# Optimization experiments

Hardware: AMD Instinct MI355X
Metric: run time of the kernel (lower is better)

## Reference

```python
import jax, jax.numpy as jnp
import numpy as np

# ---- configuration matching init_kwargs ----
CTX_C = 96        # context_v_features
M_FREQS = 8       # m_encode_num_freqs
OUT_C = 45        # out_features
NDIM = 3
SIGMA = 5.0       # sigma_encode_scale
EPS = 1e-7        # TARGET_COORD_EPSILON
CX = CY = CZ = 32
QX = QY = QZ = 48
B = 1
CTX_VOX = 2.0
Q_VOX = 1.25
N_COORD = 4 * NDIM + NDIM * 2 * M_FREQS   # 60
INTERNAL = CTX_C + N_COORD                # 156


def _lin_init(k, fi, fo):
    s = 1.0 / np.sqrt(fi)
    kw, kb = jax.random.split(k)
    return (jax.random.uniform(kw, (fi, fo), jnp.float32, -s, s),
            jax.random.uniform(kb, (fo,), jnp.float32, -s, s))


def setup_inputs() -> dict:
    key = jax.random.key(0)
    ks = jax.random.split(key, 12)
    context_v = jax.random.normal(ks[0], (B, CTX_C, CX, CY, CZ), jnp.float32)
    ax = jnp.arange(CX, dtype=jnp.float32) * CTX_VOX
    gx, gy, gz = jnp.meshgrid(ax, ax, ax, indexing='ij')
    context_spatial_extent = jnp.broadcast_to(
        jnp.stack([gx, gy, gz], 0)[None], (B, 3, CX, CY, CZ)).astype(jnp.float32)
    # queries in the interior so nearest-idx + 1 stays in bounds
    query_coord = jax.random.uniform(ks[1], (B, 3, QX, QY, QZ), jnp.float32,
                                     CTX_VOX, (CX - 2) * CTX_VOX)
    query_vox_size = jnp.full((B, 3), Q_VOX, jnp.float32)
    inp = dict(context_v=context_v, context_spatial_extent=context_spatial_extent,
               query_vox_size=query_vox_size, query_coord=query_coord)
    ki = 2
    for b in range(2):
        inp[f'blk{b}_w0'], inp[f'blk{b}_b0'] = _lin_init(ks[ki], INTERNAL, CTX_C); ki += 1
        inp[f'blk{b}_w1'], inp[f'blk{b}_b1'] = _lin_init(ks[ki], CTX_C, CTX_C); ki += 1
        inp[f'blk{b}_w2'], inp[f'blk{b}_b2'] = _lin_init(ks[ki], CTX_C, CTX_C); ki += 1
    inp['post_w'], inp['post_b'] = _lin_init(ks[ki], CTX_C, OUT_C)
    return inp


def _flat(t):
    # 'b c x y z -> (b x y z) c'
    return jnp.moveaxis(t, 1, -1).reshape(-1, t.shape[1])


def _unflat(t, b, x, y, z):
    # '(b x y z) c -> b c x y z'
    return jnp.moveaxis(t.reshape(b, x, y, z, -1), -1, 1)


def _fourier(c):
    # c: (N, 3) normalized coords; geometric frequency ladder scaled by sigma
    freqs = SIGMA ** (jnp.arange(M_FREQS, dtype=c.dtype) / M_FREQS)   # (m,)
    ang = (2.0 * jnp.pi) * c[:, :, None] * freqs                      # (N,3,m)
    return jnp.concatenate([jnp.sin(ang), jnp.cos(ang)], axis=-1).reshape(c.shape[0], -1)


def _skip_block(x, coord, w0, b0, w1, b1, w2, b2):
    # SkipMLPBlock: concat(context, coord) -> 3 dense SiLU layers -> residual add
    h = jnp.concatenate([x, coord], axis=-1)
    h = jax.nn.silu(h @ w0 + b0)
    h = jax.nn.silu(h @ w1 + b1)
    h = jax.nn.silu(h @ w2 + b2)
    return x + h, coord


def _sub_grid_forward(ctx_val, ctx_coord, q_coord, ctx_vox, q_vox, p):
    # ctx_val: (B,C,X,Y,Z); coords: (B,3,X,Y,Z); ctx_vox/q_vox: (B,3,1,1,1)
    b, _, x, y, z = q_coord.shape
    rel = jnp.maximum(ctx_coord - q_coord, -ctx_vox / 2 + EPS)
    rel_norm = (rel - jnp.min(rel, axis=(2, 3, 4), keepdims=True)) / (1.5 * ctx_vox)
    enc = _fourier(_flat(rel_norm))                                   # (N, 6m)
    qv = jnp.broadcast_to(q_vox, rel_norm.shape)
    coord_feats = jnp.concatenate(
        [_flat(qv), _flat(ctx_coord), _flat(q_coord), _flat(rel_norm), enc], axis=-1)
    h = _flat(ctx_val)
    xc = coord_feats
    for i in range(2):
        h, xc = _skip_block(h, xc, p[f'blk{i}_w0'], p[f'blk{i}_b0'],
                            p[f'blk{i}_w1'], p[f'blk{i}_b1'],
                            p[f'blk{i}_w2'], p[f'blk{i}_b2'])
    pred = h @ p['post_w'] + p['post_b']
    return _unflat(pred, b, x, y, z), rel


def reference(context_v, context_spatial_extent, query_vox_size, query_coord,
              blk0_w0, blk0_b0, blk0_w1, blk0_b1, blk0_w2, blk0_b2,
              blk1_w0, blk1_b0, blk1_w1, blk1_b1, blk1_w2, blk1_b2,
              post_w, post_b):
    p = dict(blk0_w0=blk0_w0, blk0_b0=blk0_b0, blk0_w1=blk0_w1, blk0_b1=blk0_b1,
             blk0_w2=blk0_w2, blk0_b2=blk0_b2, blk1_w0=blk1_w0, blk1_b0=blk1_b0,
             blk1_w1=blk1_w1, blk1_b1=blk1_b1, blk1_w2=blk1_w2, blk1_b2=blk1_b2,
             post_w=post_w, post_b=post_b)
    bsz, _, qx, qy, qz = query_coord.shape
    cx, cy, cz = context_spatial_extent.shape[2:]
    ctx_vox = jnp.abs(context_spatial_extent[..., 1, 1, 1]
                      - context_spatial_extent[..., 0, 0, 0])[:, :, None, None, None]
    q_vox = query_vox_size[:, :, None, None, None]
    # nearest context voxel index per query point (regular grid)
    origin = context_spatial_extent[:, :, 0, 0, 0][:, :, None, None, None]
    nearest = jnp.round((query_coord - origin) / ctx_vox).astype(jnp.int32)
    xi = jnp.clip(nearest[:, 0], 0, cx - 2).reshape(-1)
    yi = jnp.clip(nearest[:, 1], 0, cy - 2).reshape(-1)
    zi = jnp.clip(nearest[:, 2], 0, cz - 2).reshape(-1)
    b_idx = jnp.broadcast_to(jnp.arange(bsz)[:, None, None, None],
                             (bsz, qx, qy, qz)).reshape(-1)
    preds = []
    rel000 = None
    for i in (0, 1):
        for j in (0, 1):
            for k in (0, 1):
                cval = context_v[b_idx, :, xi + i, yi + j, zi + k]            # (N,C) gather
                cval = _unflat(cval, bsz, qx, qy, qz)
                ccoord = context_spatial_extent[b_idx, :, xi + i, yi + j, zi + k]
                ccoord = _unflat(ccoord, bsz, qx, qy, qz)
                pred, rel = _sub_grid_forward(cval, ccoord, query_coord,
                                              ctx_vox, q_vox, p)
                preds.append(pred)
                if i == 0 and j == 0 and k == 0:
                    rel000 = rel
    preds = jnp.stack(preds, 0)   # (8, B, OUT, X, Y, Z)
    # trilinear combine over the 2x2x2 sub-window (grid_sample align_corners=True;
    # grid coord channel 0 indexes z_sub (W), 1 -> y_sub (H), 2 -> x_sub (D))
    g = jnp.clip((rel000 - 0.5) * 2.0, -1.0 + EPS, 1.0 - EPS)
    t = (g + 1.0) / 2.0
    tz, ty, tx = t[:, 0], t[:, 1], t[:, 2]
    out = jnp.zeros_like(preds[0])
    for i in (0, 1):
        wi = tx if i == 1 else 1.0 - tx
        for j in (0, 1):
            wj = ty if j == 1 else 1.0 - ty
            for k in (0, 1):
                wk = tz if k == 1 else 1.0 - tz
                out = out + preds[i * 4 + j * 2 + k] * (wi * wj * wk)[:, None]
    return out
```

## Files before the change

kernel.cpp:

```cpp
#include <hip/hip_runtime.h>
#include <hip/hip_bf16.h>

typedef unsigned short ushort_t;
typedef short short8 __attribute__((ext_vector_type(8)));
typedef short shrt4 __attribute__((ext_vector_type(4)));
typedef unsigned short ush4 __attribute__((ext_vector_type(4)));
typedef unsigned int uintx2 __attribute__((ext_vector_type(2)));
typedef float floatx4 __attribute__((ext_vector_type(4)));

#define SA 168
#define SW 104
#define NQ 110592
#define CVOL 32768

#define L0A   0
#define L0B   15360
#define A1_00 30720
#define A1_01 39936
#define A1_10 49152
#define A1_11 58368
#define PST   67584
#define WTOT  72192
#define BTOT  9216

#define WSW_OFF  64
#define BIAS_OFF 147456
#define CVT_OFF  196608

#define TXP_NB   256
#define PREP_NB  318
#define PRE_NB   (TXP_NB + PREP_NB + 432)

#if defined(__HIP_DEVICE_COMPILE__)
#define MFMA16(A, B, C) __builtin_amdgcn_mfma_f32_16x16x16bf16_1k(A, B, C, 0, 0, 0)
#else
#define MFMA16(A, B, C) (C)
#endif

#if defined(__HIP_DEVICE_COMPILE__) && __has_builtin(__builtin_amdgcn_sinf) && __has_builtin(__builtin_amdgcn_cosf) && __has_builtin(__builtin_amdgcn_fractf)
#define FAST_SINCOS 1
#else
#define FAST_SINCOS 0
#endif

__device__ __forceinline__ float bf2f(ushort_t u) { return __uint_as_float(((unsigned)u) << 16); }
__device__ __forceinline__ ushort_t f2bf(float f) {
    unsigned u = __float_as_uint(f);
    unsigned r = (u + 0x7fffu + ((u >> 16) & 1u)) >> 16;
    return (ushort_t)r;
}
__device__ __forceinline__ unsigned pkpair(float a, float b) {
#if defined(__HIP_DEVICE_COMPILE__) && __has_builtin(__builtin_amdgcn_cvt_pk_bf16_f32)
    return __builtin_bit_cast(unsigned, __builtin_amdgcn_cvt_pk_bf16_f32(a, b));
#else
    unsigned ua = __float_as_uint(a) + 0x8000u;
    unsigned ub = __float_as_uint(b) + 0x8000u;
    return __builtin_amdgcn_perm(ub, ua, 0x07060302);
#endif
}
__device__ __forceinline__ shrt4 pk4(floatx4 v) {
    uintx2 u;
    u[0] = pkpair(v[0], v[1]);
    u[1] = pkpair(v[2], v[3]);
    return __builtin_bit_cast(shrt4, u);
}
__device__ __forceinline__ unsigned encodeMin(float x) {
    unsigned u = __float_as_uint(x);
    return (u & 0x80000000u) ? ~u : (u | 0x80000000u);
}
__device__ __forceinline__ float decodeMin(unsigned key) {
    unsigned u = (key & 0x80000000u) ? (key ^ 0x80000000u) : ~key;
    return __uint_as_float(u);
}

__device__ __constant__ float FREQ[8] = {
    1.0f, 1.2228445f, 1.4953488f, 1.8285791f,
    2.2360680f, 2.7343640f, 3.3437015f, 4.0888269f
};

__global__ void decoder_pre(const float* __restrict__ cv, ushort_t* __restrict__ cvT,
                            const float* __restrict__ w00, const float* __restrict__ b00,
                            const float* __restrict__ w01, const float* __restrict__ b01,
                            const float* __restrict__ w02, const float* __restrict__ b02,
                            const float* __restrict__ w10, const float* __restrict__ b10,
                            const float* __restrict__ w11, const float* __restrict__ b11,
                            const float* __restrict__ w12, const float* __restrict__ b12,
                            const float* __restrict__ pw, ushort_t* __restrict__ wsW,
                            float* __restrict__ biasF,
                            const float* __restrict__ qc, const float* __restrict__ ext,
                            unsigned* __restrict__ keys) {
    __shared__ ushort_t ld[128 * SW];
    __shared__ unsigned mk[3];
    const int bx = blockIdx.x;
    const int tid = threadIdx.x;

    if (bx < TXP_NB) {
        int base = bx * 128;
        int cl = tid & 127, h = tid >> 7;
        #pragma unroll 4
        for (int ch = h * 48; ch < h * 48 + 48; ++ch)
            ld[cl * SW + ch] = f2bf(cv[ch * CVOL + base + cl]);
        __syncthreads();
        #pragma unroll
        for (int it = 0; it < 6; ++it) {
            int idx = it * 256 + tid;
            int r = idx / 12, c = idx - r * 12;
            *(uint4*)&cvT[(base + r) * 96 + c * 8] = *(const uint4*)&ld[r * SW + c * 8];
        }
        return;
    }
    if (bx < TXP_NB + PREP_NB) {
        int idx = (bx - TXP_NB) * 256 + tid;
        if (idx >= WTOT + BTOT) return;
        if (idx >= WTOT) {
            int t = idx - WTOT;
            int layer = t / 1536, rem = t - layer * 1536;
            int mt = rem >> 8, l2i = rem & 255;
            int lane = l2i >> 2, r = l2i & 3;
            int m = mt * 16 + (lane >> 4) * 4 + r;
            const float* B = layer == 0 ? b00 : layer == 1 ? b01 : layer == 2 ? b02
                           : layer == 3 ? b10 : layer == 4 ? b11 : b12;
            biasF[t] = B[m];
            return;
        }
        ushort_t v = 0;
        if (idx < A1_00) {
            const float* W = (idx < L0B) ? w00 : w10;
            int li = idx - ((idx < L0B) ? L0A : L0B);
            int j = li & 7, lane = (li >> 3) & 63, chunk = li >> 9;
            int kc = chunk % 5, mt = chunk / 5;
            int k = kc * 32 + (lane >> 4) * 8 + j;
            int m = mt * 16 + (lane & 15);
            if (k < 156) v = f2bf(W[k * 96 + m]);
        } else if (idx < PST) {
            const float* W = idx < A1_01 ? w01 : idx < A1_10 ? w02 : idx < A1_11 ? w11 : w12;
            int off = idx < A1_01 ? A1_00 : idx < A1_10 ? A1_01 : idx < A1_11 ? A1_10 : A1_11;
            int li = idx - off;
            int i = li & 3, kl = (li >> 2) & 1, lane = (li >> 3) & 63, chunk = li >> 9;
            int kp = chunk % 3, mt = chunk / 3;
            int k = (kp * 2 + kl) * 16 + (lane >> 4) * 4 + i;
            int m = mt * 16 + (lane & 15);
            v = f2bf(W[k * 96 + m]);
        } else {
            int li = idx - PST;
            int j = li & 7, lane = (li >> 3) & 63, chunk = li >> 9;
            int kc = chunk % 3, t = chunk / 3;
            int k = kc * 32 + (lane >> 4) * 8 + j;
            int n = t * 16 + (lane & 15);
            if (n < 45) v = f2bf(pw[k * 45 + n]);
        }
        wsW[idx] = v;
        return;
    }
    {
        int lane = tid & 63;
        if (tid < 3) mk[tid] = 0xFFFFFFFFu;
        __syncthreads();
        int p = (bx - TXP_NB - PREP_NB) * 256 + tid;
        #pragma unroll
        for (int c = 0; c < 3; ++c) {
            float org = ext[c * CVOL];
            float vox = fabsf(ext[c * CVOL + 1057] - org);
            float q = qc[c * NQ + p];
            float nf = rintf((q - org) / vox);
            int ci = (int)nf; ci = ci < 0 ? 0 : (ci > 30 ? 30 : ci);
            float base = org + (float)ci * vox - q;
            for (int off = 32; off > 0; off >>= 1) base = fminf(base, __shfl_xor(base, off));
            if (lane == 0) atomicMin(&mk[c], encodeMin(base));
        }
        __syncthreads();
        if (tid < 3) atomicMin(&keys[tid], mk[tid]);
    }
}

__global__ __launch_bounds__(256, 3) void decoder_main(
    const ushort_t* __restrict__ cvT, const float* __restrict__ ext,
    const float* __restrict__ qvx, const float* __restrict__ qc,
    const float* __restrict__ pb, const ushort_t* __restrict__ wsW,
    const float* __restrict__ biasF,
    const unsigned* __restrict__ minKeys, float* __restrict__ out)
{
    __shared__ ushort_t Xin[128 * SA];
    __shared__ ushort_t Hhat[16 * SW];
    __shared__ float ptQ[3][16], ptBase[3][16], ptT[3][16];
    __shared__ int ptCI[3][16];
    __shared__ float wcorn[16][8];

    const int tid = threadIdx.x;
    const int lane = tid & 63;
    const int wv = tid >> 6;
    const int quad = lane >> 4;
    const int l16 = lane & 15;
    const int lane8 = lane << 3, quad8 = quad * 8, quad4 = quad * 4;
    const int p0 = blockIdx.x * 16;
    const int col0 = wv * 32;

    float vox[3], org[3], lim[3], inv3v[3], qv[3], mrel[3][2];
    #pragma unroll
    for (int c = 0; c < 3; ++c) {
        org[c] = ext[c * CVOL];
        vox[c] = fabsf(ext[c * CVOL + 1057] - org[c]);
        lim[c] = -0.5f * vox[c] + 1e-7f;
        inv3v[c] = 1.0f / (1.5f * vox[c]);
        qv[c] = qvx[c];
        float mb = decodeMin(minKeys[c]);
        mrel[c][0] = fmaxf(mb, lim[c]);
        mrel[c][1] = fmaxf(mb + vox[c], lim[c]);
    }

    if (tid < 64) {
        int p = tid >> 2, c = tid & 3;
        if (c < 3) {
            float q = qc[c * NQ + p0 + p];
            float nf = rintf((q - org[c]) / vox[c]);
            int ci = (int)nf; ci = ci < 0 ? 0 : (ci > 30 ? 30 : ci);
            float base = org[c] + (float)ci * vox[c] - q;
            float rel0 = fmaxf(base, lim[c]);
            float g = fminf(fmaxf((rel0 - 0.5f) * 2.0f, -1.0f + 1e-7f), 1.0f - 1e-7f);
            ptQ[c][p] = q; ptCI[c][p] = ci; ptBase[c][p] = base; ptT[c][p] = (g + 1.0f) * 0.5f;
        }
    }
    __syncthreads();

    if (tid < 128) {
        int p = tid >> 3, corner = tid & 7;
        int i = corner >> 2, j = (corner >> 1) & 1, k = corner & 1;
        float wx = i ? ptT[2][p] : 1.0f - ptT[2][p];
        float wy = j ? ptT[1][p] : 1.0f - ptT[1][p];
        float wz = k ? ptT[0][p] : 1.0f - ptT[0][p];
        wcorn[p][corner] = wx * wy * wz;
    }

    {
        const int r = tid >> 1, h = tid & 1;
        const int p = r >> 3, corner = r & 7;
        const int i0 = corner >> 2, i1 = (corner >> 1) & 1, i2 = corner & 1;
        int io[3] = {i0, i1, i2};

        int cell = (ptCI[0][p] + i0) * 1024 + (ptCI[1][p] + i1) * 32 + ptCI[2][p] + i2;
        const uint4* src = (const uint4*)&cvT[cell * 96];
        uint4* dstX = (uint4*)&Xin[r * SA];
        #pragma unroll
        for (int cc = h * 6; cc < h * 6 + 6; ++cc) dstX[cc] = src[cc];

        float rn[3];
        #pragma unroll
        for (int c = 0; c < 3; ++c) {
            float rel = fmaxf(ptBase[c][p] + (float)io[c] * vox[c], lim[c]);
            rn[c] = (rel - mrel[c][io[c]]) * inv3v[c];
        }
        ushort_t* row = &Xin[r * SA];
        if (h == 0) {
            #pragma unroll
            for (int c = 0; c < 3; ++c) {
                row[96 + c]  = f2bf(qv[c]);
                row[99 + c]  = f2bf(org[c] + (float)(ptCI[c][p] + io[c]) * vox[c]);
                row[102 + c] = f2bf(ptQ[c][p]);
                row[105 + c] = f2bf(rn[c]);
            }
            #pragma unroll
            for (int z = 156; z < SA; ++z) row[z] = 0;
            #pragma unroll
            for (int m = 0; m < 8; ++m) {
                float ang = rn[0] * FREQ[m];
#if FAST_SINCOS
                float fr = __builtin_amdgcn_fractf(ang);
                row[108 + m] = f2bf(__builtin_amdgcn_sinf(fr));
                row[116 + m] = f2bf(__builtin_amdgcn_cosf(fr));
#else
                float s, co; sincospif(2.0f * ang, &s, &co);
                row[108 + m] = f2bf(s); row[116 + m] = f2bf(co);
#endif
            }
        } else {
            #pragma unroll
            for (int c = 1; c < 3; ++c) {
                #pragma unroll
                for (int m = 0; m < 8; ++m) {
                    float ang = rn[c] * FREQ[m];
#if FAST_SINCOS
                    float fr = __builtin_amdgcn_fractf(ang);
                    row[108 + c * 16 + m] = f2bf(__builtin_amdgcn_sinf(fr));
                    row[108 + c * 16 + 8 + m] = f2bf(__builtin_amdgcn_cosf(fr));
#else
                    float s, co; sincospif(2.0f * ang, &s, &co);
                    row[108 + c * 16 + m] = f2bf(s);
                    row[108 + c * 16 + 8 + m] = f2bf(co);
#endif
                }
            }
        }
    }
    __syncthreads();

    const int A32off[2] = {L0A, L0B};
    const int A16off[2][2] = {{A1_00, A1_01}, {A1_10, A1_11}};
    floatx4 acc[6][2];
    shrt4 bfr[6][2];

    #pragma unroll
    for (int blk = 0; blk < 2; ++blk) {
        {
            short8 bX[2][5];
            #pragma unroll
            for (int nt = 0; nt < 2; ++nt)
                #pragma unroll
                for (int kc = 0; kc < 5; ++kc)
                    bX[nt][kc] = *(const short8*)&Xin[(col0 + nt * 16 + l16) * SA + kc * 32 + quad8];
            const int lay = blk * 3;
            #pragma unroll
            for (int mt = 0; mt < 6; ++mt) {
                short8 aw[5];
                #pragma unroll
                for (int kc = 0; kc < 5; ++kc)
                    aw[kc] = *(const short8*)&wsW[A32off[blk] + ((mt * 5 + kc) << 9) + lane8];
                floatx4 bv = *(const floatx4*)&biasF[((lay * 6 + mt) << 8) + (lane << 2)];
                #pragma unroll
                for (int nt = 0; nt < 2; ++nt) {
                    floatx4 a = __builtin_amdgcn_mfma_f32_16x16x32_bf16(aw[0], bX[nt][0], bv, 0, 0, 0);
                    #pragma unroll
                    for (int kc = 1; kc < 5; ++kc)
                        a = __builtin_amdgcn_mfma_f32_16x16x32_bf16(aw[kc], bX[nt][kc], a, 0, 0, 0);
                    acc[mt][nt] = a;
                }
            }
        }
        {
            #pragma unroll
            for (int mt = 0; mt < 6; ++mt)
                #pragma unroll
                for (int nt = 0; nt < 2; ++nt) {
                    floatx4 s;
                    #pragma unroll
                    for (int r = 0; r < 4; ++r) {
                        float z = acc[mt][nt][r];
                        s[r] = z * __builtin_amdgcn_rcpf(1.0f + __expf(-z));
                    }
                    bfr[mt][nt] = pk4(s);
                }
        }
        #pragma unroll
        for (int l = 1; l < 3; ++l) {
            const int lay = blk * 3 + l;
            #pragma unroll
            for (int mt = 0; mt < 6; ++mt) {
                short8 awp[3];
                #pragma unroll
                for (int kp = 0; kp < 3; ++kp)
                    awp[kp] = *(const short8*)&wsW[A16off[blk][l - 1] + ((mt * 3 + kp) << 9) + lane8];
                floatx4 bv = *(const floatx4*)&biasF[((lay * 6 + mt) << 8) + (lane << 2)];
                #pragma unroll
                for (int nt = 0; nt < 2; ++nt) {
                    shrt4 a0 = __builtin_shufflevector(awp[0], awp[0], 0, 1, 2, 3);
                    floatx4 a = MFMA16(a0, bfr[0][nt], bv);
                    #pragma unroll
                    for (int kc = 1; kc < 6; ++kc) {
                        shrt4 af = (kc & 1)
                            ? __builtin_shufflevector(awp[kc >> 1], awp[kc >> 1], 4, 5, 6, 7)
                            : __builtin_shufflevector(awp[kc >> 1], awp[kc >> 1], 0, 1, 2, 3);
                        a = MFMA16(af, bfr[kc][nt], a);
                    }
                    acc[mt][nt] = a;
                }
            }
            if (l == 1) {
                #pragma unroll
                for (int mt = 0; mt < 6; ++mt)
                    #pragma unroll
                    for (int nt = 0; nt < 2; ++nt) {
                        floatx4 s;
                        #pragma unroll
                        for (int r = 0; r < 4; ++r) {
                            float z = acc[mt][nt][r];
                            s[r] = z * __builtin_amdgcn_rcpf(1.0f + __expf(-z));
                        }
                        bfr[mt][nt] = pk4(s);
                    }
            } else {
                #pragma unroll
                for (int mt = 0; mt < 6; ++mt)
                    #pragma unroll
                    for (int nt = 0; nt < 2; ++nt) {
                        int ca = (col0 + nt * 16 + l16) * SA + mt * 16 + quad4;
                        ush4 hu = *(const ush4*)&Xin[ca];
                        floatx4 s;
                        #pragma unroll
                        for (int r = 0; r < 4; ++r) {
                            float z = acc[mt][nt][r];
                            s[r] = z * __builtin_amdgcn_rcpf(1.0f + __expf(-z)) + bf2f(hu[r]);
                        }
                        uintx2 w;
                        w[0] = pkpair(s[0], s[1]);
                        w[1] = pkpair(s[2], s[3]);
                        *(uintx2*)&Xin[ca] = w;
                    }
            }
        }
    }

    {
        int p = tid >> 4, s6 = (tid & 15) * 6;
        float w8[8];
        #pragma unroll
        for (int c = 0; c < 8; ++c) w8[c] = wcorn[p][c];
        float sum[6] = {0.f, 0.f, 0.f, 0.f, 0.f, 0.f};
        #pragma unroll
        for (int c = 0; c < 8; ++c) {
            const unsigned* rp = (const unsigned*)&Xin[(p * 8 + c) * SA + s6];
            float w = w8[c];
            #pragma unroll
            for (int d = 0; d < 3; ++d) {
                unsigned u = rp[d];
                sum[d * 2]     += w * __uint_as_float(u << 16);
                sum[d * 2 + 1] += w * __uint_as_float(u & 0xFFFF0000u);
            }
        }
        unsigned* hp = (unsigned*)&Hhat[p * SW + s6];
        #pragma unroll
        for (int d = 0; d < 3; ++d) hp[d] = pkpair(sum[d * 2], sum[d * 2 + 1]);
    }
    __syncthreads();

    if (wv < 3) {
        const ushort_t* wb = wsW + PST;
        floatx4 pacc = {0.f, 0.f, 0.f, 0.f};
        #pragma unroll
        for (int kc = 0; kc < 3; ++kc) {
            short8 a = *(const short8*)&Hhat[l16 * SW + kc * 32 + quad8];
            short8 bfrag = *(const short8*)&wb[((wv * 3 + kc) << 9) + lane8];
            pacc = __builtin_amdgcn_mfma_f32_16x16x32_bf16(a, bfrag, pacc, 0, 0, 0);
        }
        int n = 16 * wv + l16;
        if (n < 45) {
            float bv = pb[n];
            float4 v;
            v.x = pacc[0] + bv; v.y = pacc[1] + bv; v.z = pacc[2] + bv; v.w = pacc[3] + bv;
            *(float4*)&out[n * NQ + p0 + quad * 4] = v;
        }
    }
}

extern "C" void kernel_launch(void* const* d_in, const int* in_sizes, int n_in,
                              void* d_out, int out_size, void* d_ws, size_t ws_size,
                              hipStream_t stream) {
    (void)in_sizes; (void)n_in; (void)out_size; (void)ws_size;
    const float* cv  = (const float*)d_in[0];
    const float* ext = (const float*)d_in[1];
    const float* qvx = (const float*)d_in[2];
    const float* qc  = (const float*)d_in[3];
    const float* w00 = (const float*)d_in[4];
    const float* b00 = (const float*)d_in[5];
    const float* w01 = (const float*)d_in[6];
    const float* b01 = (const float*)d_in[7];
    const float* w02 = (const float*)d_in[8];
    const float* b02 = (const float*)d_in[9];
    const float* w10 = (const float*)d_in[10];
    const float* b10 = (const float*)d_in[11];
    const float* w11 = (const float*)d_in[12];
    const float* b11 = (const float*)d_in[13];
    const float* w12 = (const float*)d_in[14];
    const float* b12 = (const float*)d_in[15];
    const float* pw  = (const float*)d_in[16];
    const float* pb  = (const float*)d_in[17];

    unsigned* keys = (unsigned*)d_ws;
    ushort_t* wsW  = (ushort_t*)((char*)d_ws + WSW_OFF);
    float* biasF   = (float*)((char*)d_ws + BIAS_OFF);
    ushort_t* cvT  = (ushort_t*)((char*)d_ws + CVT_OFF);

    hipMemsetAsync(keys, 0xFF, 12, stream);
    decoder_pre<<<PRE_NB, 256, 0, stream>>>(cv, cvT,
                                            w00, b00, w01, b01, w02, b02,
                                            w10, b10, w11, b11, w12, b12,
                                            pw, wsW, biasF, qc, ext, keys);
    decoder_main<<<6912, 256, 0, stream>>>(cvT, ext, qvx, qc,
                                           pb, wsW, biasF, keys, (float*)d_out);
}
```

Measured before the change: 323.9 us.

## Compute coordinate/Fourier features directly into MFMA B-fragment registers

```diff
diff --git a/kernel.cpp b/kernel.cpp
--- a/kernel.cpp
+++ b/kernel.cpp
@@ -6,9 +6,10 @@
 typedef short shrt4 __attribute__((ext_vector_type(4)));
 typedef unsigned short ush4 __attribute__((ext_vector_type(4)));
 typedef unsigned int uintx2 __attribute__((ext_vector_type(2)));
+typedef unsigned int uintx4 __attribute__((ext_vector_type(4)));
 typedef float floatx4 __attribute__((ext_vector_type(4)));
 
-#define SA 168
+#define SA 104
 #define SW 104
 #define NQ 110592
 #define CVOL 32768
@@ -64,6 +65,14 @@
     u[1] = pkpair(v[2], v[3]);
     return __builtin_bit_cast(shrt4, u);
 }
+__device__ __forceinline__ short8 pk8(const float (&v)[8]) {
+    uintx4 u;
+    u[0] = pkpair(v[0], v[1]);
+    u[1] = pkpair(v[2], v[3]);
+    u[2] = pkpair(v[4], v[5]);
+    u[3] = pkpair(v[6], v[7]);
+    return __builtin_bit_cast(short8, u);
+}
 __device__ __forceinline__ unsigned encodeMin(float x) {
     unsigned u = __float_as_uint(x);
     return (u & 0x80000000u) ? ~u : (u | 0x80000000u);
@@ -73,7 +82,26 @@
     return __uint_as_float(u);
 }
 
+__device__ __forceinline__ float sin_r(float ang) {
+#if FAST_SINCOS
+    return __builtin_amdgcn_sinf(__builtin_amdgcn_fractf(ang));
+#else
+    float s, c; sincospif(2.0f * ang, &s, &c); return s;
+#endif
+}
+__device__ __forceinline__ float cos_r(float ang) {
+#if FAST_SINCOS
+    return __builtin_amdgcn_cosf(__builtin_amdgcn_fractf(ang));
+#else
+    float s, c; sincospif(2.0f * ang, &s, &c); return c;
+#endif
+}
+
 __device__ __constant__ float FREQ[8] = {
+    1.0f, 1.2228445f, 1.4953488f, 1.8285791f,
+    2.2360680f, 2.7343640f, 3.3437015f, 4.0888269f
+};
+constexpr float FREQH[8] = {
     1.0f, 1.2228445f, 1.4953488f, 1.8285791f,
     2.2360680f, 2.7343640f, 3.3437015f, 4.0888269f
 };
@@ -173,7 +201,7 @@
     }
 }
 
-__global__ __launch_bounds__(256, 3) void decoder_main(
+__global__ __launch_bounds__(256, 4) void decoder_main(
     const ushort_t* __restrict__ cvT, const float* __restrict__ ext,
     const float* __restrict__ qvx, const float* __restrict__ qc,
     const float* __restrict__ pb, const ushort_t* __restrict__ wsW,
@@ -235,61 +263,64 @@
         const int r = tid >> 1, h = tid & 1;
         const int p = r >> 3, corner = r & 7;
         const int i0 = corner >> 2, i1 = (corner >> 1) & 1, i2 = corner & 1;
-        int io[3] = {i0, i1, i2};
-
         int cell = (ptCI[0][p] + i0) * 1024 + (ptCI[1][p] + i1) * 32 + ptCI[2][p] + i2;
         const uint4* src = (const uint4*)&cvT[cell * 96];
         uint4* dstX = (uint4*)&Xin[r * SA];
         #pragma unroll
         for (int cc = h * 6; cc < h * 6 + 6; ++cc) dstX[cc] = src[cc];
-
-        float rn[3];
+    }
+
+    short8 bF3[2], bF4[2];
+    #pragma unroll
+    for (int nt = 0; nt < 2; ++nt) {
+        const int r = col0 + nt * 16 + l16;
+        const int p = r >> 3, corner = r & 7;
+        const int io[3] = {corner >> 2, (corner >> 1) & 1, corner & 1};
+        float rn[3], cc3[3], qp[3];
         #pragma unroll
         for (int c = 0; c < 3; ++c) {
             float rel = fmaxf(ptBase[c][p] + (float)io[c] * vox[c], lim[c]);
             rn[c] = (rel - mrel[c][io[c]]) * inv3v[c];
-        }
-        ushort_t* row = &Xin[r * SA];
-        if (h == 0) {
-            #pragma unroll
-            for (int c = 0; c < 3; ++c) {
-                row[96 + c]  = f2bf(qv[c]);
-                row[99 + c]  = f2bf(org[c] + (float)(ptCI[c][p] + io[c]) * vox[c]);
-                row[102 + c] = f2bf(ptQ[c][p]);
-                row[105 + c] = f2bf(rn[c]);
-            }
-            #pragma unroll
-            for (int z = 156; z < SA; ++z) row[z] = 0;
-            #pragma unroll
-            for (int m = 0; m < 8; ++m) {
-                float ang = rn[0] * FREQ[m];
-#if FAST_SINCOS
-                float fr = __builtin_amdgcn_fractf(ang);
-                row[108 + m] = f2bf(__builtin_amdgcn_sinf(fr));
-                row[116 + m] = f2bf(__builtin_amdgcn_cosf(fr));
-#else
-                float s, co; sincospif(2.0f * ang, &s, &co);
-                row[108 + m] = f2bf(s); row[116 + m] = f2bf(co);
-#endif
-            }
+            cc3[c] = org[c] + (float)(ptCI[c][p] + io[c]) * vox[c];
+            qp[c] = ptQ[c][p];
+        }
+        float fa[8], fb[8];
+        if (quad == 0) {
+            fa[0] = qv[0]; fa[1] = qv[1]; fa[2] = qv[2];
+            fa[3] = cc3[0]; fa[4] = cc3[1]; fa[5] = cc3[2];
+            fa[6] = qp[0]; fa[7] = qp[1];
+            #pragma unroll
+            for (int m = 0; m < 4; ++m) fb[m]     = sin_r(rn[1] * FREQH[4 + m]);
+            #pragma unroll
+            for (int m = 0; m < 4; ++m) fb[4 + m] = cos_r(rn[1] * FREQH[m]);
+        } else if (quad == 1) {
+            fa[0] = qp[2]; fa[1] = rn[0]; fa[2] = rn[1]; fa[3] = rn[2];
+            #pragma unroll
+            for (int m = 0; m < 4; ++m) fa[4 + m] = sin_r(rn[0] * FREQH[m]);
+            #pragma unroll
+            for (int m = 0; m < 4; ++m) fb[m]     = cos_r(rn[1] * FREQH[4 + m]);
+            #pragma unroll
+            for (int m = 0; m < 4; ++m) fb[4 + m] = sin_r(rn[2] * FREQH[m]);
+        } else if (quad == 2) {
+            #pragma unroll
+            for (int m = 0; m < 4; ++m) fa[m]     = sin_r(rn[0] * FREQH[4 + m]);
+            #pragma unroll
+            for (int m = 0; m < 4; ++m) fa[4 + m] = cos_r(rn[0] * FREQH[m]);
+            #pragma unroll
+            for (int m = 0; m < 4; ++m) fb[m]     = sin_r(rn[2] * FREQH[4 + m]);
+            #pragma unroll
+            for (int m = 0; m < 4; ++m) fb[4 + m] = cos_r(rn[2] * FREQH[m]);
         } else {
             #pragma unroll
-            for (int c = 1; c < 3; ++c) {
-                #pragma unroll
-                for (int m = 0; m < 8; ++m) {
-                    float ang = rn[c] * FREQ[m];
-#if FAST_SINCOS
-                    float fr = __builtin_amdgcn_fractf(ang);
-                    row[108 + c * 16 + m] = f2bf(__builtin_amdgcn_sinf(fr));
-                    row[108 + c * 16 + 8 + m] = f2bf(__builtin_amdgcn_cosf(fr));
-#else
-                    float s, co; sincospif(2.0f * ang, &s, &co);
-                    row[108 + c * 16 + m] = f2bf(s);
-                    row[108 + c * 16 + 8 + m] = f2bf(co);
-#endif
-                }
-            }
-        }
+            for (int m = 0; m < 4; ++m) fa[m]     = cos_r(rn[0] * FREQH[4 + m]);
+            #pragma unroll
+            for (int m = 0; m < 4; ++m) fa[4 + m] = sin_r(rn[1] * FREQH[m]);
+            #pragma unroll
+            for (int m = 0; m < 4; ++m) fb[m]     = cos_r(rn[2] * FREQH[4 + m]);
+            fb[4] = 0.f; fb[5] = 0.f; fb[6] = 0.f; fb[7] = 0.f;
+        }
+        bF3[nt] = pk8(fa);
+        bF4[nt] = pk8(fb);
     }
     __syncthreads();
 
@@ -301,11 +332,11 @@
     #pragma unroll
     for (int blk = 0; blk < 2; ++blk) {
         {
-            short8 bX[2][5];
+            short8 bX[2][3];
             #pragma unroll
             for (int nt = 0; nt < 2; ++nt)
                 #pragma unroll
-                for (int kc = 0; kc < 5; ++kc)
+                for (int kc = 0; kc < 3; ++kc)
                     bX[nt][kc] = *(const short8*)&Xin[(col0 + nt * 16 + l16) * SA + kc * 32 + quad8];
             const int lay = blk * 3;
             #pragma unroll
@@ -318,9 +349,10 @@
                 #pragma unroll
                 for (int nt = 0; nt < 2; ++nt) {
                     floatx4 a = __builtin_amdgcn_mfma_f32_16x16x32_bf16(aw[0], bX[nt][0], bv, 0, 0, 0);
-                    #pragma unroll
-                    for (int kc = 1; kc < 5; ++kc)
-                        a = __builtin_amdgcn_mfma_f32_16x16x32_bf16(aw[kc], bX[nt][kc], a, 0, 0, 0);
+                    a = __builtin_amdgcn_mfma_f32_16x16x32_bf16(aw[1], bX[nt][1], a, 0, 0, 0);
+                    a = __builtin_amdgcn_mfma_f32_16x16x32_bf16(aw[2], bX[nt][2], a, 0, 0, 0);
+                    a = __builtin_amdgcn_mfma_f32_16x16x32_bf16(aw[3], bF3[nt], a, 0, 0, 0);
+                    a = __builtin_amdgcn_mfma_f32_16x16x32_bf16(aw[4], bF4[nt], a, 0, 0, 0);
                     acc[mt][nt] = a;
                 }
             }
```

Result: no change. 328.8 us (+1.5%).
